# Kernel optimization log

Measured on AMD Instinct MI355X. Metric: run time of the kernel, lower is better.

The kernel has to match this reference:

```python
import jax, jax.numpy as jnp
import numpy as np

N_NODES, N_EDGES, N_GRAPHS, EMB_DIM, IMG_DIM, N_TYPES = 50000, 800000, 64, 128, 4096, 30


def gcn_conv(x, W, b, row, col, ew, dis, n):
    # PyG GCNConv: x @ W.T, symmetric-normalized weighted aggregation with self-loops, + bias
    xw = x @ W.T                                            # [N, D]
    norm = dis[row] * ew * dis[col]                          # [E]
    agg = jax.ops.segment_sum(norm[:, None] * xw[row], col, num_segments=n)
    agg = agg + (dis * dis)[:, None] * xw                    # self-loop (weight 1) term
    return agg + b


def setup_inputs() -> dict:
    key = jax.random.key(0)
    ks = jax.random.split(key, 20)
    inp = {
        "images": jax.random.normal(ks[0], (N_GRAPHS, IMG_DIM), jnp.float32),
        "node_types": jax.random.randint(ks[1], (N_NODES,), 0, N_TYPES),
        "edge_index": jax.random.randint(ks[2], (2, N_EDGES), 0, N_NODES),
        "edge_attr": jax.random.uniform(ks[3], (N_EDGES,), jnp.float32),
        "batch": jnp.sort(jax.random.randint(ks[4], (N_NODES,), 0, N_GRAPHS)),
    }
    def lin(k, out_d, in_d):
        s = 1.0 / np.sqrt(in_d)
        kw, kb = jax.random.split(k)
        return (jax.random.uniform(kw, (out_d, in_d), jnp.float32, -s, s),
                jax.random.uniform(kb, (out_d,), jnp.float32, -s, s))
    inp["emb_table"] = jax.random.normal(ks[5], (N_TYPES, EMB_DIM), jnp.float32)
    inp["W_img"], inp["b_img"] = lin(ks[6], IMG_DIM, IMG_DIM)      # frozen image backbone head
    inp["W1"], inp["b1"] = lin(ks[7], EMB_DIM, EMB_DIM)
    inp["W2"], inp["b2"] = lin(ks[8], EMB_DIM, EMB_DIM)
    inp["W3"], inp["b3"] = lin(ks[9], EMB_DIM, EMB_DIM)
    inp["Wi"], inp["bi"] = lin(ks[10], EMB_DIM, IMG_DIM)
    inp["Wc"], inp["bc"] = lin(ks[11], EMB_DIM, IMG_DIM + EMB_DIM)
    return inp


def reference(images, node_types, edge_index, edge_attr, batch, emb_table,
              W_img, b_img, W1, b1, W2, b2, W3, b3, Wi, bi, Wc, bc):
    n = node_types.shape[0]
    B = images.shape[0]
    row, col = edge_index[0], edge_index[1]
    # gcn_norm with self-loops (fill value 1): deg at aggregation endpoint (col)
    deg = jax.ops.segment_sum(edge_attr, col, num_segments=n) + 1.0
    dis = jax.lax.rsqrt(deg)
    # frozen image model (linear stand-in for VGG fc head, output dim 4096)
    xi = images @ W_img.T + b_img                           # [B, 4096]
    # encode_images branch
    oi = xi @ Wi.T + bi
    oi = oi / jnp.linalg.norm(oi, axis=1, keepdims=True)
    # encode_images_with_graphs branch
    xg = emb_table[node_types]                              # [N, D]
    xg = jax.nn.relu(gcn_conv(xg, W1, b1, row, col, edge_attr, dis, n))
    xg = jax.nn.relu(gcn_conv(xg, W2, b2, row, col, edge_attr, dis, n))
    xg = gcn_conv(xg, W3, b3, row, col, edge_attr, dis, n)
    cnt = jax.ops.segment_sum(jnp.ones((n,), xg.dtype), batch, num_segments=B)
    pooled = jax.ops.segment_sum(xg, batch, num_segments=B) / jnp.maximum(cnt, 1.0)[:, None]
    oc = jnp.concatenate([xi, pooled], axis=1) @ Wc.T + bc
    oc = oc / jnp.linalg.norm(oc, axis=1, keepdims=True)
    return (oi, oc)
```

## Files before the change

### kernel.cpp

```cpp
#include <hip/hip_runtime.h>
#include <math.h>

#define NN 50000
#define NE 800000
#define NG 64
#define D 128
#define IMG 4096
#define NT 30
#define CAP 48
#define PART 196
#define PCAP 6144
#define GSTRIDE 16

#define PABLK ((NE + 1023) / 1024)
#define PBLK ((NT * D + 2 * D * 64) / 256)
#define GBLK ((NN + 63) / 64)
#define AGGBLK ((NN + 7) / 8)
#define KSPLIT 16
#define IMGALL (64 * KSPLIT)
#define IREDBLK (64 * IMG / 256)
#define SRCMASK 0x1FFFF

typedef unsigned int uint;
typedef unsigned short ushort;
typedef __attribute__((ext_vector_type(8))) __bf16 bf16x8;
typedef __attribute__((ext_vector_type(4))) float f32x4;

__device__ __forceinline__ uint bf16rne(float f) {
  uint h = __float_as_uint(f);
  return (h + 0x7fffu + ((h >> 16) & 1u)) >> 16;
}
__device__ __forceinline__ uint pack2bf(float a, float b) {
  return bf16rne(a) | (bf16rne(b) << 16);
}
__device__ __forceinline__ float bflo(uint u) { return __uint_as_float(u << 16); }
__device__ __forceinline__ float bfhi(uint u) { return __uint_as_float(u & 0xffff0000u); }



__device__ __forceinline__ void img_mfma_body(const float* __restrict__ A,
                                              const float* __restrict__ W,
                                              float* __restrict__ splitbuf, int bx, int by) {
  int wv = threadIdx.x >> 6, lane = threadIdx.x & 63;
  int quad = lane >> 4;
  int n = bx * 64 + wv * 16 + (lane & 15);
  int k0 = by * 256;
  f32x4 acc[4] = {{0.f, 0.f, 0.f, 0.f}, {0.f, 0.f, 0.f, 0.f},
                  {0.f, 0.f, 0.f, 0.f}, {0.f, 0.f, 0.f, 0.f}};
  const float* wp = W + (size_t)n * IMG + k0 + quad * 16;
  const float* ap = A + (size_t)(lane & 15) * IMG + k0 + quad * 16;
  #pragma unroll
  for (int ss = 0; ss < 4; ss++) {
    float4 w0 = *(const float4*)(wp + ss * 64);
    float4 w1 = *(const float4*)(wp + ss * 64 + 4);
    float4 w2 = *(const float4*)(wp + ss * 64 + 8);
    float4 w3 = *(const float4*)(wp + ss * 64 + 12);
    union { uint4 u; bf16x8 v; } b1u, b2u;
    b1u.u.x = pack2bf(w0.x, w0.y);
    b1u.u.y = pack2bf(w0.z, w0.w);
    b1u.u.z = pack2bf(w1.x, w1.y);
    b1u.u.w = pack2bf(w1.z, w1.w);
    b2u.u.x = pack2bf(w2.x, w2.y);
    b2u.u.y = pack2bf(w2.z, w2.w);
    b2u.u.z = pack2bf(w3.x, w3.y);
    b2u.u.w = pack2bf(w3.z, w3.w);
    #pragma unroll
    for (int mt = 0; mt < 4; mt++) {
      const float* app = ap + (size_t)mt * 16 * IMG + ss * 64;
      float4 a0_ = *(const float4*)(app);
      float4 a1_ = *(const float4*)(app + 4);
      float4 a2_ = *(const float4*)(app + 8);
      float4 a3_ = *(const float4*)(app + 12);
      union { uint4 u; bf16x8 v; } a1u, a2u;
      a1u.u.x = pack2bf(a0_.x, a0_.y);
      a1u.u.y = pack2bf(a0_.z, a0_.w);
      a1u.u.z = pack2bf(a1_.x, a1_.y);
      a1u.u.w = pack2bf(a1_.z, a1_.w);
      a2u.u.x = pack2bf(a2_.x, a2_.y);
      a2u.u.y = pack2bf(a2_.z, a2_.w);
      a2u.u.z = pack2bf(a3_.x, a3_.y);
      a2u.u.w = pack2bf(a3_.z, a3_.w);
      acc[mt] = __builtin_amdgcn_mfma_f32_16x16x32_bf16(a1u.v, b1u.v, acc[mt], 0, 0, 0);
      acc[mt] = __builtin_amdgcn_mfma_f32_16x16x32_bf16(a2u.v, b2u.v, acc[mt], 0, 0, 0);
    }
  }
  #pragma unroll
  for (int mt = 0; mt < 4; mt++)
    #pragma unroll
    for (int i = 0; i < 4; i++) {
      int m = mt * 16 + quad * 4 + i;
      splitbuf[((size_t)by * 64 + m) * IMG + n] = acc[mt][i];
    }
}


__global__ __launch_bounds__(256) void setup_fused(
    const int* __restrict__ row, const int* __restrict__ col,
    const float* __restrict__ ew, int* __restrict__ gbase, int2* __restrict__ pedge,
    const float* __restrict__ emb, const float* __restrict__ W1, float* __restrict__ embW,
    const float* __restrict__ W2, const float* __restrict__ W3,
    uint* __restrict__ Wbf2, uint* __restrict__ Wbf3,
    const float* __restrict__ images, const float* __restrict__ Wimg,
    float* __restrict__ splitbuf,
    const int* __restrict__ batch, int* __restrict__ goff) {
  __shared__ int sh[2 * PART];
  int b = blockIdx.x;
  if (b < IMGALL) {
    img_mfma_body(images, Wimg, splitbuf, b & 63, b >> 6);
  } else if (b < IMGALL + PABLK) {
    int* hist = sh;
    int* lbase = sh + PART;
    int t = threadIdx.x;
    for (int i = t; i < 2 * PART; i += 256) sh[i] = 0;
    __syncthreads();
    int e0 = (b - IMGALL) * 1024 + t * 4;
    int4 c4, r4;
    float4 w4;
    int pt0 = 0, pt1 = 0, pt2 = 0, pt3 = 0;
    int s0 = 0, s1 = 0, s2 = 0, s3 = 0;
    bool act = e0 < NE;
    if (act) {
      c4 = *(const int4*)(col + e0);
      r4 = *(const int4*)(row + e0);
      w4 = *(const float4*)(ew + e0);
      pt0 = c4.x >> 8; pt1 = c4.y >> 8; pt2 = c4.z >> 8; pt3 = c4.w >> 8;
      s0 = atomicAdd(&hist[pt0], 1);
      s1 = atomicAdd(&hist[pt1], 1);
      s2 = atomicAdd(&hist[pt2], 1);
      s3 = atomicAdd(&hist[pt3], 1);
    }
    __syncthreads();
    for (int i = t; i < PART; i += 256) {
      int c = hist[i];
      lbase[i] = c ? atomicAdd(&gbase[i * GSTRIDE], c) : 0;
    }
    __syncthreads();
    if (act) {
      int i0 = lbase[pt0] + s0;
      int i1 = lbase[pt1] + s1;
      int i2 = lbase[pt2] + s2;
      int i3 = lbase[pt3] + s3;
      if (i0 < PCAP)
        pedge[(size_t)pt0 * PCAP + i0] = make_int2(r4.x | ((c4.x & 255) << 17),
                                                   __float_as_int(w4.x));
      if (i1 < PCAP)
        pedge[(size_t)pt1 * PCAP + i1] = make_int2(r4.y | ((c4.y & 255) << 17),
                                                   __float_as_int(w4.y));
      if (i2 < PCAP)
        pedge[(size_t)pt2 * PCAP + i2] = make_int2(r4.z | ((c4.z & 255) << 17),
                                                   __float_as_int(w4.z));
      if (i3 < PCAP)
        pedge[(size_t)pt3 * PCAP + i3] = make_int2(r4.w | ((c4.w & 255) << 17),
                                                   __float_as_int(w4.w));
    }
  } else if (b < IMGALL + PABLK + PBLK) {
    int tid = (b - IMGALL - PABLK) * 256 + threadIdx.x;
    if (tid < NT * D) {
      int tt = tid >> 7, nn2 = tid & 127;
      const float* ep = emb + (size_t)tt * D;
      const float* wp = W1 + (size_t)nn2 * D;
      float acc = 0.f;
      for (int k = 0; k < D; k += 4) {
        float4 evv = *(const float4*)(ep + k);
        float4 wvv = *(const float4*)(wp + k);
        acc += evv.x * wvv.x + evv.y * wvv.y + evv.z * wvv.z + evv.w * wvv.w;
      }
      embW[tid] = acc;
    } else if (tid < NT * D + D * 64) {
      int j = tid - NT * D;
      float2 v = ((const float2*)W2)[j];
      Wbf2[j] = pack2bf(v.x, v.y);
    } else {
      int j = tid - NT * D - D * 64;
      float2 v = ((const float2*)W3)[j];
      Wbf3[j] = pack2bf(v.x, v.y);
    }
  } else {
    int g = threadIdx.x;
    if (g <= NG) {
      int lo = 0, hi = NN;
      while (lo < hi) {
        int mid = (lo + hi) >> 1;
        if (batch[mid] < g) lo = mid + 1; else hi = mid;
      }
      goff[g] = lo;
    }
  }
}


__global__ __launch_bounds__(256) void bucket_build(const int* __restrict__ gbase,
                                                    const int2* __restrict__ pedge,
                                                    const int* __restrict__ types,
                                                    int2* __restrict__ ebuf,
                                                    int* __restrict__ cnt,
                                                    float* __restrict__ dis) {
  __shared__ int lcnt[256];
  __shared__ float ldeg[256];
  int t = threadIdx.x;
  lcnt[t] = 0;
  ldeg[t] = 0.f;
  __syncthreads();
  int p = blockIdx.x;
  int total = min(gbase[p * GSTRIDE], PCAP);
  const int2* src = pedge + (size_t)p * PCAP;
  for (int i = t; i < total; i += 256) {
    int2 rec = src[i];
    int nl = (rec.x >> 17) & 255;
    int sv = rec.x & SRCMASK;
    int s = atomicAdd(&lcnt[nl], 1);
    atomicAdd(&ldeg[nl], __int_as_float(rec.y));
    if (s < CAP)
      ebuf[(size_t)(p * 256 + nl) * CAP + s] = make_int2(sv | (types[sv] << 17), rec.y);
  }
  __syncthreads();
  int node = p * 256 + t;
  if (node < NN) {
    cnt[node] = lcnt[t];
    dis[node] = 1.0f / sqrtf(ldeg[t] + 1.0f);
  }
}


__global__ __launch_bounds__(512) void lay1_fused(const int* __restrict__ cnt,
                                                  const int2* __restrict__ ebuf,
                                                  const float* __restrict__ dis,
                                                  const int* __restrict__ types,
                                                  const float* __restrict__ embW,
                                                  const float* __restrict__ b1,
                                                  uint* __restrict__ outbf) {
  __shared__ float sE[NT * D];
  __shared__ float sB[D];
  int t = threadIdx.x;
  for (int i = t; i < NT * D; i += 512) sE[i] = embW[i];
  if (t < D) sB[t] = b1[t];
  __syncthreads();
  int wave = t >> 6, lane = t & 63;
  #pragma unroll
  for (int r = 0; r < 4; r++) {
    int node = blockIdx.x * 32 + wave * 4 + r;
    if (node >= NN) continue;
    float ax = sB[2 * lane], ay = sB[2 * lane + 1];
    int n = min(cnt[node], CAP);
    int nc = (n + 7) >> 3;
    const int2* eb = ebuf + (size_t)node * CAP;
    float disc = dis[node];
    for (int c = 0; c < nc; c++) {
      const int2* ep = eb + (c << 3);
      int4 q0 = *(const int4*)(ep + 0);
      int4 q1 = *(const int4*)(ep + 2);
      int4 q2 = *(const int4*)(ep + 4);
      int4 q3 = *(const int4*)(ep + 6);
      int t0 = q0.x >> 17, t1 = q0.z >> 17, t2 = q1.x >> 17, t3 = q1.z >> 17;
      int t4 = q2.x >> 17, t5 = q2.z >> 17, t6 = q3.x >> 17, t7 = q3.z >> 17;
      float m0 = dis[q0.x & SRCMASK] * __int_as_float(q0.y) * disc;
      float m1 = dis[q0.z & SRCMASK] * __int_as_float(q0.w) * disc;
      float m2 = dis[q1.x & SRCMASK] * __int_as_float(q1.y) * disc;
      float m3 = dis[q1.z & SRCMASK] * __int_as_float(q1.w) * disc;
      float m4 = dis[q2.x & SRCMASK] * __int_as_float(q2.y) * disc;
      float m5 = dis[q2.z & SRCMASK] * __int_as_float(q2.w) * disc;
      float m6 = dis[q3.x & SRCMASK] * __int_as_float(q3.y) * disc;
      float m7 = dis[q3.z & SRCMASK] * __int_as_float(q3.w) * disc;
      float2 e0 = *(const float2*)&sE[t0 * D + 2 * lane];
      float2 e1 = *(const float2*)&sE[t1 * D + 2 * lane];
      float2 e2 = *(const float2*)&sE[t2 * D + 2 * lane];
      float2 e3 = *(const float2*)&sE[t3 * D + 2 * lane];
      float2 e4 = *(const float2*)&sE[t4 * D + 2 * lane];
      float2 e5 = *(const float2*)&sE[t5 * D + 2 * lane];
      float2 e6 = *(const float2*)&sE[t6 * D + 2 * lane];
      float2 e7 = *(const float2*)&sE[t7 * D + 2 * lane];
      ax = fmaf(m0, e0.x, ax); ay = fmaf(m0, e0.y, ay);
      ax = fmaf(m1, e1.x, ax); ay = fmaf(m1, e1.y, ay);
      ax = fmaf(m2, e2.x, ax); ay = fmaf(m2, e2.y, ay);
      ax = fmaf(m3, e3.x, ax); ay = fmaf(m3, e3.y, ay);
      ax = fmaf(m4, e4.x, ax); ay = fmaf(m4, e4.y, ay);
      ax = fmaf(m5, e5.x, ax); ay = fmaf(m5, e5.y, ay);
      ax = fmaf(m6, e6.x, ax); ay = fmaf(m6, e6.y, ay);
      ax = fmaf(m7, e7.x, ax); ay = fmaf(m7, e7.y, ay);
    }
    float dd = disc * disc;
    float2 es = *(const float2*)&sE[types[node] * D + 2 * lane];
    ax = fmaf(dd, es.x, ax);
    ay = fmaf(dd, es.y, ay);
    ax = fmaxf(ax, 0.f);
    ay = fmaxf(ay, 0.f);
    outbf[(size_t)node * 64 + lane] = pack2bf(ax, ay);
  }
}


__device__ __forceinline__ void node_gemm_body(const uint* __restrict__ Abf,
                                               const uint* __restrict__ Wbf,
                                               uint* __restrict__ outbf, int bx,
                                               ushort* __restrict__ tile) {
  int w = threadIdx.x >> 6, lane = threadIdx.x & 63;
  int quad = lane >> 4;
  int m0 = bx * 64 + w * 16;
  int mrow = m0 + (lane & 15);
  int arow = (mrow < NN) ? mrow : 0;
  uint4 afr[4];
  #pragma unroll
  for (int ks = 0; ks < 4; ks++)
    afr[ks] = *(const uint4*)(Abf + (size_t)arow * 64 + ks * 16 + quad * 4);
  f32x4 acc[8] = {};
  #pragma unroll
  for (int nt = 0; nt < 8; nt++) {
    int n = nt * 16 + (lane & 15);
    #pragma unroll
    for (int ks = 0; ks < 4; ks++) {
      union { uint4 u; bf16x8 v; } au, bu;
      au.u = afr[ks];
      bu.u = *(const uint4*)(Wbf + (size_t)n * 64 + ks * 16 + quad * 4);
      acc[nt] = __builtin_amdgcn_mfma_f32_16x16x32_bf16(au.v, bu.v, acc[nt], 0, 0, 0);
    }
  }
  ushort* tw = tile + w * 16 * 136;
  #pragma unroll
  for (int nt = 0; nt < 8; nt++)
    #pragma unroll
    for (int i = 0; i < 4; i++)
      tw[(quad * 4 + i) * 136 + nt * 16 + (lane & 15)] = (ushort)bf16rne(acc[nt][i]);
  __builtin_amdgcn_s_waitcnt(0);
  #pragma unroll
  for (int rep = 0; rep < 4; rep++) {
    int r = rep * 4 + quad;
    int j = lane & 15;
    int node = m0 + r;
    if (node < NN) {
      uint4 v = *(const uint4*)&tw[r * 136 + j * 8];
      *(uint4*)(outbf + (size_t)node * 64 + j * 4) = v;
    }
  }
}


#define GA(k, s_) uint2 u##k = xw2[(size_t)(s_) * 32 + fl];
#define FA(k, m_) a0 = fmaf(m_, bflo(u##k.x), a0); a1 = fmaf(m_, bfhi(u##k.x), a1); \
                  a2 = fmaf(m_, bflo(u##k.y), a2); a3 = fmaf(m_, bfhi(u##k.y), a3);

__device__ __forceinline__ void aggregate2_body(const uint* __restrict__ xw,
                                                const int* __restrict__ cnt,
                                                const int2* __restrict__ ebuf,
                                                const float* __restrict__ dis,
                                                const float* __restrict__ bias, int relu,
                                                uint* __restrict__ outbf, int blk) {
  const uint2* xw2 = (const uint2*)xw;
  int wave = threadIdx.x >> 6;
  int lane = threadIdx.x & 63;
  int half = lane >> 5;
  int fl = lane & 31;
  int node = (blk * 4 + wave) * 2 + half;
  if (node >= NN) return;
  float a0 = 0.f, a1 = 0.f, a2 = 0.f, a3 = 0.f;
  int n = min(cnt[node], CAP);
  int nc = (n + 15) >> 4;
  const int2* eb = ebuf + (size_t)node * CAP;
  float disc = dis[node];
  for (int c = 0; c < nc; c++) {
    const int2* ep = eb + (c << 4);
    int4 r0 = *(const int4*)(ep + 0);
    int4 r1 = *(const int4*)(ep + 2);
    int4 r2 = *(const int4*)(ep + 4);
    int4 r3 = *(const int4*)(ep + 6);
    int4 r4 = *(const int4*)(ep + 8);
    int4 r5 = *(const int4*)(ep + 10);
    int4 r6 = *(const int4*)(ep + 12);
    int4 r7 = *(const int4*)(ep + 14);
    int s0 = r0.x & SRCMASK, s1 = r0.z & SRCMASK, s2 = r1.x & SRCMASK, s3 = r1.z & SRCMASK;
    int s4 = r2.x & SRCMASK, s5 = r2.z & SRCMASK, s6 = r3.x & SRCMASK, s7 = r3.z & SRCMASK;
    int s8 = r4.x & SRCMASK, s9 = r4.z & SRCMASK, s10 = r5.x & SRCMASK, s11 = r5.z & SRCMASK;
    int s12 = r6.x & SRCMASK, s13 = r6.z & SRCMASK, s14 = r7.x & SRCMASK, s15 = r7.z & SRCMASK;
    GA(0, s0)  GA(1, s1)  GA(2, s2)  GA(3, s3)
    GA(4, s4)  GA(5, s5)  GA(6, s6)  GA(7, s7)
    GA(8, s8)  GA(9, s9)  GA(10, s10) GA(11, s11)
    GA(12, s12) GA(13, s13) GA(14, s14) GA(15, s15)
    float m0 = dis[s0] * __int_as_float(r0.y) * disc;
    float m1 = dis[s1] * __int_as_float(r0.w) * disc;
    float m2 = dis[s2] * __int_as_float(r1.y) * disc;
    float m3 = dis[s3] * __int_as_float(r1.w) * disc;
    float m4 = dis[s4] * __int_as_float(r2.y) * disc;
    float m5 = dis[s5] * __int_as_float(r2.w) * disc;
    float m6 = dis[s6] * __int_as_float(r3.y) * disc;
    float m7 = dis[s7] * __int_as_float(r3.w) * disc;
    float m8 = dis[s8] * __int_as_float(r4.y) * disc;
    float m9 = dis[s9] * __int_as_float(r4.w) * disc;
    float m10 = dis[s10] * __int_as_float(r5.y) * disc;
    float m11 = dis[s11] * __int_as_float(r5.w) * disc;
    float m12 = dis[s12] * __int_as_float(r6.y) * disc;
    float m13 = dis[s13] * __int_as_float(r6.w) * disc;
    float m14 = dis[s14] * __int_as_float(r7.y) * disc;
    float m15 = dis[s15] * __int_as_float(r7.w) * disc;
    FA(0, m0)  FA(1, m1)  FA(2, m2)  FA(3, m3)
    FA(4, m4)  FA(5, m5)  FA(6, m6)  FA(7, m7)
    FA(8, m8)  FA(9, m9)  FA(10, m10) FA(11, m11)
    FA(12, m12) FA(13, m13) FA(14, m14) FA(15, m15)
  }
  float dd = disc * disc;
  {
    uint2 u = xw2[(size_t)node * 32 + fl];
    a0 = fmaf(dd, bflo(u.x), a0);
    a1 = fmaf(dd, bfhi(u.x), a1);
    a2 = fmaf(dd, bflo(u.y), a2);
    a3 = fmaf(dd, bfhi(u.y), a3);
  }
  float4 b = *(const float4*)(bias + 4 * fl);
  a0 += b.x; a1 += b.y; a2 += b.z; a3 += b.w;
  if (relu) {
    a0 = fmaxf(a0, 0.f);
    a1 = fmaxf(a1, 0.f);
    a2 = fmaxf(a2, 0.f);
    a3 = fmaxf(a3, 0.f);
  }
  uint2 o;
  o.x = pack2bf(a0, a1);
  o.y = pack2bf(a2, a3);
  ((uint2*)outbf)[(size_t)node * 32 + fl] = o;
}


__device__ __forceinline__ void gemm64_body(const float* __restrict__ A, int lda,
                                            const float* __restrict__ W,
                                            const float* __restrict__ bias,
                                            float* __restrict__ out, int N, int K,
                                            int kChunk, int bx, int by,
                                            float (*xs)[68], float (*ws)[68]) {
  int t = threadIdx.x;
  int n0 = bx * 64;
  int k0 = by * kChunk;
  int kEnd = min(K, k0 + kChunk);
  int tn = t & 15;
  int tm = t >> 4;
  float acc[4][4] = {};
  if (by == 0) {
    #pragma unroll
    for (int ni = 0; ni < 4; ni++) {
      float bv = bias[n0 + tn * 4 + ni];
      #pragma unroll
      for (int mi = 0; mi < 4; mi++) acc[mi][ni] = bv;
    }
  }
  for (int kt = k0; kt < kEnd; kt += 16) {
    int kc = (t & 3) * 4;
    int rr = t >> 2;
    float4 va = *(const float4*)(A + (size_t)rr * lda + kt + kc);
    xs[kc + 0][rr] = va.x; xs[kc + 1][rr] = va.y; xs[kc + 2][rr] = va.z; xs[kc + 3][rr] = va.w;
    float4 vw = *(const float4*)(W + (size_t)(n0 + rr) * K + kt + kc);
    ws[kc + 0][rr] = vw.x; ws[kc + 1][rr] = vw.y; ws[kc + 2][rr] = vw.z; ws[kc + 3][rr] = vw.w;
    __syncthreads();
    #pragma unroll
    for (int k = 0; k < 16; k++) {
      float4 xv = *(const float4*)&xs[k][tm * 4];
      float4 wv = *(const float4*)&ws[k][tn * 4];
      float xm[4] = {xv.x, xv.y, xv.z, xv.w};
      float wn[4] = {wv.x, wv.y, wv.z, wv.w};
      #pragma unroll
      for (int mi = 0; mi < 4; mi++)
        #pragma unroll
        for (int ni = 0; ni < 4; ni++)
          acc[mi][ni] = fmaf(xm[mi], wn[ni], acc[mi][ni]);
    }
    __syncthreads();
  }
  #pragma unroll
  for (int mi = 0; mi < 4; mi++)
    #pragma unroll
    for (int ni = 0; ni < 4; ni++)
      atomicAdd(&out[(size_t)(tm * 4 + mi) * N + n0 + tn * 4 + ni], acc[mi][ni]);
}

__global__ __launch_bounds__(256) void gemm2_plus_imgred(const uint* __restrict__ bufX,
                                                         const uint* __restrict__ wbf2,
                                                         uint* __restrict__ bufB,
                                                         const float* __restrict__ splitbuf,
                                                         const float* __restrict__ b_img,
                                                         float* __restrict__ xcat) {
  __shared__ ushort tile[4 * 16 * 136];
  int b = blockIdx.x;
  if (b < IREDBLK) {
    int idx = b * 256 + threadIdx.x;
    float acc = b_img[idx & (IMG - 1)];
    #pragma unroll
    for (int s = 0; s < KSPLIT; s++) acc += splitbuf[(size_t)s * 64 * IMG + idx];
    xcat[(size_t)(idx >> 12) * (IMG + D) + (idx & (IMG - 1))] = acc;
  } else {
    node_gemm_body(bufX, wbf2, bufB, b - IREDBLK, tile);
  }
}

__global__ __launch_bounds__(256) void aggregate2(const uint* __restrict__ xw,
                                                  const int* __restrict__ cnt,
                                                  const int2* __restrict__ ebuf,
                                                  const float* __restrict__ dis,
                                                  const float* __restrict__ bias, int relu,
                                                  uint* __restrict__ outbf) {
  aggregate2_body(xw, cnt, ebuf, dis, bias, relu, outbf, blockIdx.x);
}

__global__ __launch_bounds__(256) void gemm3_plus_oi(const uint* __restrict__ bufX,
                                                     const uint* __restrict__ wbf3,
                                                     uint* __restrict__ bufB,
                                                     const float* __restrict__ xcat,
                                                     const float* __restrict__ Wi,
                                                     const float* __restrict__ bi,
                                                     float* __restrict__ oi_raw) {
  __shared__ __align__(16) char smem[4 * 16 * 136 * 2];
  int b = blockIdx.x;
  if (b < 64) {
    float (*xs)[68] = (float(*)[68])smem;
    float (*ws)[68] = (float(*)[68])(smem + 16 * 68 * 4);
    gemm64_body(xcat, IMG + D, Wi, bi, oi_raw, D, IMG, 128, b & 1, b >> 1, xs, ws);
  } else {
    node_gemm_body(bufX, wbf3, bufB, b - 64, (ushort*)smem);
  }
}

__global__ __launch_bounds__(256) void agg3_plus_ocmain(const uint* __restrict__ bufB,
                                                        const int* __restrict__ cnt,
                                                        const int2* __restrict__ ebuf,
                                                        const float* __restrict__ dis,
                                                        const float* __restrict__ b3,
                                                        uint* __restrict__ bufX,
                                                        const float* __restrict__ xcat,
                                                        const float* __restrict__ Wc,
                                                        const float* __restrict__ bc,
                                                        float* __restrict__ oc_raw) {
  __shared__ float xs[16][68];
  __shared__ float ws[16][68];
  int b = blockIdx.x;
  if (b < 64) {
    gemm64_body(xcat, IMG + D, Wc, bc, oc_raw, D, IMG + D, 128, b & 1, b >> 1, xs, ws);
  } else {
    aggregate2_body(bufB, cnt, ebuf, dis, b3, 0, bufX, b - 64);
  }
}


__global__ __launch_bounds__(64) void pool_bf(const uint* __restrict__ xb,
                                              const int* __restrict__ goff,
                                              float* __restrict__ xcat) {
  int g = blockIdx.x >> 5;
  int chunk = blockIdx.x & 31;
  int fl = threadIdx.x;
  int s = goff[g], e = goff[g + 1];
  float inv = 1.0f / fmaxf((float)(e - s), 1.0f);
  float ax = 0.f, ay = 0.f;
  for (int i = s + chunk; i < e; i += 32) {
    uint u = xb[(size_t)i * 64 + fl];
    ax += bflo(u);
    ay += bfhi(u);
  }
  atomicAdd(&xcat[(size_t)g * (IMG + D) + IMG + 2 * fl], ax * inv);
  atomicAdd(&xcat[(size_t)g * (IMG + D) + IMG + 2 * fl + 1], ay * inv);
}

__global__ __launch_bounds__(256) void oc_tail(const float* __restrict__ xcat,
                                               const float* __restrict__ Wc,
                                               const float* __restrict__ bc,
                                               float* __restrict__ oc_raw) {
  __shared__ float xs[16][68];
  __shared__ float ws[16][68];
  gemm64_body(xcat, IMG + D, Wc, bc, oc_raw, D, IMG + D, 4096, blockIdx.x, 1, xs, ws);
}

__global__ __launch_bounds__(128) void normalize_rows(const float* __restrict__ oi_raw,
                                                      const float* __restrict__ oc_raw,
                                                      float* __restrict__ out) {
  int r = blockIdx.x;
  int t = threadIdx.x;
  const float* src = (r < 64) ? (oi_raw + r * D) : (oc_raw + (r - 64) * D);
  float v = src[t];
  __shared__ float red[128];
  red[t] = v * v;
  __syncthreads();
  for (int s = 64; s > 0; s >>= 1) {
    if (t < s) red[t] += red[t + s];
    __syncthreads();
  }
  out[r * D + t] = v / sqrtf(red[0]);
}


extern "C" void kernel_launch(void* const* d_in, const int* in_sizes, int n_in,
                              void* d_out, int out_size, void* d_ws, size_t ws_size,
                              hipStream_t stream) {
  const float* images = (const float*)d_in[0];
  const int* node_types = (const int*)d_in[1];
  const int* erow = (const int*)d_in[2];
  const int* ecol = erow + NE;
  const float* eattr = (const float*)d_in[3];
  const int* batch = (const int*)d_in[4];
  const float* emb = (const float*)d_in[5];
  const float* W_img = (const float*)d_in[6];
  const float* b_img = (const float*)d_in[7];
  const float* W1 = (const float*)d_in[8];
  const float* b1 = (const float*)d_in[9];
  const float* W2 = (const float*)d_in[10];
  const float* b2 = (const float*)d_in[11];
  const float* W3 = (const float*)d_in[12];
  const float* b3 = (const float*)d_in[13];
  const float* Wi = (const float*)d_in[14];
  const float* bi = (const float*)d_in[15];
  const float* Wc = (const float*)d_in[16];
  const float* bc = (const float*)d_in[17];
  float* out = (float*)d_out;

  char* w = (char*)d_ws;
  auto alloc = [&](size_t bytes) -> void* {
    void* p = (void*)w;
    w += (bytes + 511) & ~(size_t)511;
    return p;
  };
  int* gbase = (int*)alloc((size_t)PART * GSTRIDE * 4);
  float* xcat = (float*)alloc((size_t)64 * (IMG + D) * 4);
  float* oi_raw = (float*)alloc(64 * D * 4);
  float* oc_raw = (float*)alloc(64 * D * 4);
  int2* ebuf = (int2*)alloc((size_t)NN * CAP * 8);
  size_t zero_bytes = (size_t)(w - (char*)d_ws);
  int* cnt = (int*)alloc((size_t)NN * 4);
  int* goff = (int*)alloc((NG + 1) * 4);
  float* dis = (float*)alloc(NN * 4);
  float* embW1 = (float*)alloc(NT * D * 4);
  uint* wbf2 = (uint*)alloc(D * 64 * 4);
  uint* wbf3 = (uint*)alloc(D * 64 * 4);
  int2* pedge = (int2*)alloc((size_t)PART * PCAP * 8);
  uint* bufX = (uint*)alloc((size_t)NN * D * 2);
  uint* bufB = (uint*)alloc((size_t)NN * D * 2);
  float* splitbuf = (float*)alloc((size_t)KSPLIT * 64 * IMG * 4);

  hipMemsetAsync(d_ws, 0, zero_bytes, stream);

  setup_fused<<<IMGALL + PABLK + PBLK + 1, 256, 0, stream>>>(
      erow, ecol, eattr, gbase, pedge, emb, W1, embW1, W2, W3, wbf2, wbf3,
      images, W_img, splitbuf, batch, goff);
  bucket_build<<<PART, 256, 0, stream>>>(gbase, pedge, node_types, ebuf, cnt, dis);
  lay1_fused<<<(NN + 31) / 32, 512, 0, stream>>>(cnt, ebuf, dis, node_types, embW1, b1, bufX);
  gemm2_plus_imgred<<<IREDBLK + GBLK, 256, 0, stream>>>(bufX, wbf2, bufB, splitbuf, b_img,
                                                        xcat);
  aggregate2<<<AGGBLK, 256, 0, stream>>>(bufB, cnt, ebuf, dis, b2, 1, bufX);
  gemm3_plus_oi<<<64 + GBLK, 256, 0, stream>>>(bufX, wbf3, bufB, xcat, Wi, bi, oi_raw);
  agg3_plus_ocmain<<<64 + AGGBLK, 256, 0, stream>>>(bufB, cnt, ebuf, dis, b3, bufX,
                                                    xcat, Wc, bc, oc_raw);
  pool_bf<<<NG * 32, 64, 0, stream>>>(bufX, goff, xcat);
  oc_tail<<<2, 256, 0, stream>>>(xcat, Wc, bc, oc_raw);
  normalize_rows<<<128, 128, 0, stream>>>(oi_raw, oc_raw, out);
}
```

Before: 383.8 us.

## Pre-pack image activations to bf16 and move image GEMM into bucket kernel

Adds a small pre-pass in setup_fused that converts the 64x4096 image matrix to bf16 in the exact MFMA fragment layout. The split-K image GEMM now reads these pre-packed fragments instead of reloading and converting fp32 images in each of its 1024 blocks. The GEMM blocks also move from setup_fused into the bucket-build kernel, so they overlap with bucketing instead of with edge partitioning. This adds a small buffer and a dependency of the GEMM on the pre-pass.

```diff
diff --git a/kernel.cpp b/kernel.cpp
--- a/kernel.cpp
+++ b/kernel.cpp
@@ -14,6 +14,7 @@
 
 #define PABLK ((NE + 1023) / 1024)
 #define PBLK ((NT * D + 2 * D * 64) / 256)
+#define AFBLK 64
 #define GBLK ((NN + 63) / 64)
 #define AGGBLK ((NN + 7) / 8)
 #define KSPLIT 16
@@ -37,8 +38,10 @@
 __device__ __forceinline__ float bfhi(uint u) { return __uint_as_float(u & 0xffff0000u); }
 
 
-
-__device__ __forceinline__ void img_mfma_body(const float* __restrict__ A,
+#define AFPLANE 16384
+
+
+__device__ __forceinline__ void img_mfma_body(const uint4* __restrict__ AF,
                                               const float* __restrict__ W,
                                               float* __restrict__ splitbuf, int bx, int by) {
   int wv = threadIdx.x >> 6, lane = threadIdx.x & 63;
@@ -48,7 +51,8 @@
   f32x4 acc[4] = {{0.f, 0.f, 0.f, 0.f}, {0.f, 0.f, 0.f, 0.f},
                   {0.f, 0.f, 0.f, 0.f}, {0.f, 0.f, 0.f, 0.f}};
   const float* wp = W + (size_t)n * IMG + k0 + quad * 16;
-  const float* ap = A + (size_t)(lane & 15) * IMG + k0 + quad * 16;
+  const uint4* af0 = AF;
+  const uint4* af1 = AF + AFPLANE;
   #pragma unroll
   for (int ss = 0; ss < 4; ss++) {
     float4 w0 = *(const float4*)(wp + ss * 64);
@@ -64,22 +68,12 @@
     b2u.u.y = pack2bf(w2.z, w2.w);
     b2u.u.z = pack2bf(w3.x, w3.y);
     b2u.u.w = pack2bf(w3.z, w3.w);
+    int base = ((by * 4 + ss) * 4 + quad) * 64 + (lane & 15);
     #pragma unroll
     for (int mt = 0; mt < 4; mt++) {
-      const float* app = ap + (size_t)mt * 16 * IMG + ss * 64;
-      float4 a0_ = *(const float4*)(app);
-      float4 a1_ = *(const float4*)(app + 4);
-      float4 a2_ = *(const float4*)(app + 8);
-      float4 a3_ = *(const float4*)(app + 12);
       union { uint4 u; bf16x8 v; } a1u, a2u;
-      a1u.u.x = pack2bf(a0_.x, a0_.y);
-      a1u.u.y = pack2bf(a0_.z, a0_.w);
-      a1u.u.z = pack2bf(a1_.x, a1_.y);
-      a1u.u.w = pack2bf(a1_.z, a1_.w);
-      a2u.u.x = pack2bf(a2_.x, a2_.y);
-      a2u.u.y = pack2bf(a2_.z, a2_.w);
-      a2u.u.z = pack2bf(a3_.x, a3_.y);
-      a2u.u.w = pack2bf(a3_.z, a3_.w);
+      a1u.u = af0[base + mt * 16];
+      a2u.u = af1[base + mt * 16];
       acc[mt] = __builtin_amdgcn_mfma_f32_16x16x32_bf16(a1u.v, b1u.v, acc[mt], 0, 0, 0);
       acc[mt] = __builtin_amdgcn_mfma_f32_16x16x32_bf16(a2u.v, b2u.v, acc[mt], 0, 0, 0);
     }
@@ -100,20 +94,17 @@
     const float* __restrict__ emb, const float* __restrict__ W1, float* __restrict__ embW,
     const float* __restrict__ W2, const float* __restrict__ W3,
     uint* __restrict__ Wbf2, uint* __restrict__ Wbf3,
-    const float* __restrict__ images, const float* __restrict__ Wimg,
-    float* __restrict__ splitbuf,
+    const float* __restrict__ images, uint4* __restrict__ AF,
     const int* __restrict__ batch, int* __restrict__ goff) {
   __shared__ int sh[2 * PART];
   int b = blockIdx.x;
-  if (b < IMGALL) {
-    img_mfma_body(images, Wimg, splitbuf, b & 63, b >> 6);
-  } else if (b < IMGALL + PABLK) {
+  if (b < PABLK) {
     int* hist = sh;
     int* lbase = sh + PART;
     int t = threadIdx.x;
     for (int i = t; i < 2 * PART; i += 256) sh[i] = 0;
     __syncthreads();
-    int e0 = (b - IMGALL) * 1024 + t * 4;
+    int e0 = b * 1024 + t * 4;
     int4 c4, r4;
     float4 w4;
     int pt0 = 0, pt1 = 0, pt2 = 0, pt3 = 0;
@@ -153,8 +144,8 @@
         pedge[(size_t)pt3 * PCAP + i3] = make_int2(r4.w | ((c4.w & 255) << 17),
                                                    __float_as_int(w4.w));
     }
-  } else if (b < IMGALL + PABLK + PBLK) {
-    int tid = (b - IMGALL - PABLK) * 256 + threadIdx.x;
+  } else if (b < PABLK + PBLK) {
+    int tid = (b - PABLK) * 256 + threadIdx.x;
     if (tid < NT * D) {
       int tt = tid >> 7, nn2 = tid & 127;
       const float* ep = emb + (size_t)tt * D;
@@ -175,6 +166,28 @@
       float2 v = ((const float2*)W3)[j];
       Wbf3[j] = pack2bf(v.x, v.y);
     }
+  } else if (b < PABLK + PBLK + AFBLK) {
+    int tid2 = (b - PABLK - PBLK) * 256 + threadIdx.x;
+    int m = tid2 & 63;
+    int oo = tid2 >> 6;
+    int quad = oo & 3, ss = (oo >> 2) & 3, byy = oo >> 4;
+    int k = (byy * 16 + ss * 4 + quad) << 4;
+    const float* ap = images + (size_t)m * IMG + k;
+    float4 a0_ = *(const float4*)(ap);
+    float4 a1_ = *(const float4*)(ap + 4);
+    float4 a2_ = *(const float4*)(ap + 8);
+    float4 a3_ = *(const float4*)(ap + 12);
+    uint4 h0, h1;
+    h0.x = pack2bf(a0_.x, a0_.y);
+    h0.y = pack2bf(a0_.z, a0_.w);
+    h0.z = pack2bf(a1_.x, a1_.y);
+    h0.w = pack2bf(a1_.z, a1_.w);
+    h1.x = pack2bf(a2_.x, a2_.y);
+    h1.y = pack2bf(a2_.z, a2_.w);
+    h1.z = pack2bf(a3_.x, a3_.y);
+    h1.w = pack2bf(a3_.z, a3_.w);
+    AF[tid2] = h0;
+    AF[AFPLANE + tid2] = h1;
   } else {
     int g = threadIdx.x;
     if (g <= NG) {
@@ -189,35 +202,43 @@
 }
 
 
-__global__ __launch_bounds__(256) void bucket_build(const int* __restrict__ gbase,
-                                                    const int2* __restrict__ pedge,
-                                                    const int* __restrict__ types,
-                                                    int2* __restrict__ ebuf,
-                                                    int* __restrict__ cnt,
-                                                    float* __restrict__ dis) {
+__global__ __launch_bounds__(256) void bucket_plus_img(const int* __restrict__ gbase,
+                                                       const int2* __restrict__ pedge,
+                                                       const int* __restrict__ types,
+                                                       int2* __restrict__ ebuf,
+                                                       int* __restrict__ cnt,
+                                                       float* __restrict__ dis,
+                                                       const uint4* __restrict__ AF,
+                                                       const float* __restrict__ Wimg,
+                                                       float* __restrict__ splitbuf) {
   __shared__ int lcnt[256];
   __shared__ float ldeg[256];
-  int t = threadIdx.x;
-  lcnt[t] = 0;
-  ldeg[t] = 0.f;
-  __syncthreads();
-  int p = blockIdx.x;
-  int total = min(gbase[p * GSTRIDE], PCAP);
-  const int2* src = pedge + (size_t)p * PCAP;
-  for (int i = t; i < total; i += 256) {
-    int2 rec = src[i];
-    int nl = (rec.x >> 17) & 255;
-    int sv = rec.x & SRCMASK;
-    int s = atomicAdd(&lcnt[nl], 1);
-    atomicAdd(&ldeg[nl], __int_as_float(rec.y));
-    if (s < CAP)
-      ebuf[(size_t)(p * 256 + nl) * CAP + s] = make_int2(sv | (types[sv] << 17), rec.y);
-  }
-  __syncthreads();
-  int node = p * 256 + t;
-  if (node < NN) {
-    cnt[node] = lcnt[t];
-    dis[node] = 1.0f / sqrtf(ldeg[t] + 1.0f);
+  int b = blockIdx.x;
+  if (b < IMGALL) {
+    img_mfma_body(AF, Wimg, splitbuf, b & 63, b >> 6);
+  } else {
+    int t = threadIdx.x;
+    lcnt[t] = 0;
+    ldeg[t] = 0.f;
+    __syncthreads();
+    int p = b - IMGALL;
+    int total = min(gbase[p * GSTRIDE], PCAP);
+    const int2* src = pedge + (size_t)p * PCAP;
+    for (int i = t; i < total; i += 256) {
+      int2 rec = src[i];
+      int nl = (rec.x >> 17) & 255;
+      int sv = rec.x & SRCMASK;
+      int s = atomicAdd(&lcnt[nl], 1);
+      atomicAdd(&ldeg[nl], __int_as_float(rec.y));
+      if (s < CAP)
+        ebuf[(size_t)(p * 256 + nl) * CAP + s] = make_int2(sv | (types[sv] << 17), rec.y);
+    }
+    __syncthreads();
+    int node = p * 256 + t;
+    if (node < NN) {
+      cnt[node] = lcnt[t];
+      dis[node] = 1.0f / sqrtf(ldeg[t] + 1.0f);
+    }
   }
 }
 
@@ -623,16 +644,18 @@
   uint* wbf2 = (uint*)alloc(D * 64 * 4);
   uint* wbf3 = (uint*)alloc(D * 64 * 4);
   int2* pedge = (int2*)alloc((size_t)PART * PCAP * 8);
+  uint4* AF = (uint4*)alloc((size_t)2 * AFPLANE * 16);
   uint* bufX = (uint*)alloc((size_t)NN * D * 2);
   uint* bufB = (uint*)alloc((size_t)NN * D * 2);
   float* splitbuf = (float*)alloc((size_t)KSPLIT * 64 * IMG * 4);
 
   hipMemsetAsync(d_ws, 0, zero_bytes, stream);
 
-  setup_fused<<<IMGALL + PABLK + PBLK + 1, 256, 0, stream>>>(
+  setup_fused<<<PABLK + PBLK + AFBLK + 1, 256, 0, stream>>>(
       erow, ecol, eattr, gbase, pedge, emb, W1, embW1, W2, W3, wbf2, wbf3,
-      images, W_img, splitbuf, batch, goff);
-  bucket_build<<<PART, 256, 0, stream>>>(gbase, pedge, node_types, ebuf, cnt, dis);
+      images, AF, batch, goff);
+  bucket_plus_img<<<IMGALL + PART, 256, 0, stream>>>(gbase, pedge, node_types, ebuf,
+                                                     cnt, dis, AF, W_img, splitbuf);
   lay1_fused<<<(NN + 31) / 32, 512, 0, stream>>>(cnt, ebuf, dis, node_types, embW1, b1, bufX);
   gemm2_plus_imgred<<<IREDBLK + GBLK, 256, 0, stream>>>(bufX, wbf2, bufB, splitbuf, b_img,
                                                         xcat);
```

New measurement: 379.2 us. About the same (-1.2%).
